# Kernel optimization log

Measured on AMD Instinct MI355X. Metric: run time of the kernel, lower is better.

Reference implementation:

```python
import jax, jax.numpy as jnp
import numpy as np

B, L, H, C = 1, 512, 1024, 2


def setup_inputs() -> dict:
    key = jax.random.key(0)
    k1, k2, k3 = jax.random.split(key, 3)
    lm_output = jax.random.normal(k1, (B, L, H), dtype=jnp.float32)
    # torch Linear weight layout: [out_features, in_features]
    W1 = jax.random.normal(k2, (H, 2 * H), dtype=jnp.float32) * 0.02
    b1 = jnp.zeros((H,), dtype=jnp.float32)
    W2 = jax.random.normal(k3, (C, H), dtype=jnp.float32) * 0.02
    b2 = jnp.zeros((C,), dtype=jnp.float32)
    return {"lm_output": lm_output, "W1": W1, "b1": b1, "W2": W2, "b2": b2}


def reference(lm_output, W1, b1, W2, b2):
    # pair_emb[b,i,j] = concat(lm_output[b,j], lm_output[b,i])
    # Linear(concat(a,b)) decomposes: split W1 into the halves acting on each part.
    Wa = W1[:, :H]  # acts on lm_output_a (the j / column token)
    Wb = W1[:, H:]  # acts on lm_output_b (the i / row token)
    a_proj = jnp.einsum('blh,oh->blo', lm_output, Wa)  # [B,L,H]
    b_proj = jnp.einsum('blh,oh->blo', lm_output, Wb)  # [B,L,H]
    # hidden[b,i,j] = tanh(a_proj[b,j] + b_proj[b,i] + b1)   -> [B,L,L,H]
    hidden = jnp.tanh(a_proj[:, None, :, :] + b_proj[:, :, None, :] + b1)
    # Dropout is identity at inference time.
    logits = jnp.einsum('bijh,ch->bijc', hidden, W2) + b2  # [B,L,L,C]
    logits = (logits + jnp.swapaxes(logits, 1, 2)) / 2.0
    return logits
```

## Files before the change

kernel.cpp:

```cpp
#include <hip/hip_runtime.h>
#include <hip/hip_bf16.h>

#define HH 1024
#define LL 512
#define NT 16
#define NTRI 136

typedef __attribute__((ext_vector_type(8))) short bf16x8;
typedef __attribute__((ext_vector_type(4))) float f32x4;

static constexpr float C_EXP = 2.8853900817779268f;

static __device__ __forceinline__ uint4 pack8(float4 a, float4 b) {
    union { uint4 u; __hip_bfloat162 h[4]; } r;
    r.h[0] = __float22bfloat162_rn(make_float2(a.x, a.y));
    r.h[1] = __float22bfloat162_rn(make_float2(a.z, a.w));
    r.h[2] = __float22bfloat162_rn(make_float2(b.x, b.y));
    r.h[3] = __float22bfloat162_rn(make_float2(b.z, b.w));
    return r.u;
}

__global__ __launch_bounds__(256) void convert_kernel(
    const float* __restrict__ lm, const float* __restrict__ W1,
    const float* __restrict__ W2,
    ushort* __restrict__ lm16, ushort* __restrict__ B16, float* __restrict__ wsum)
{
    const int b = blockIdx.x;
    if (b == 1280) {
        const int tid = threadIdx.x;
        if (tid < 128) {
            const int c = tid >> 6, l = tid & 63;
            float s = 0.f;
            for (int q = l; q < 256; q += 64) {
                const float4 v = *(const float4*)&W2[c * HH + q * 4];
                s += v.x + v.y + v.z + v.w;
            }
#pragma unroll
            for (int off = 32; off; off >>= 1) s += __shfl_down(s, off, 64);
            if (l == 0) wsum[c] = s;
        }
        return;
    }
    const int q = b * 256 + threadIdx.x;
    if (q < 65536) {
        const float4 a = *(const float4*)&lm[q * 8];
        const float4 c = *(const float4*)&lm[q * 8 + 4];
        ((uint4*)lm16)[q] = pack8(a, c);
    } else {
        const int p = q - 65536;
        const int n = p >> 7, k8 = (p & 127) * 8;
        const float* src = &W1[(n & 1023) * 2048 + (n >> 10) * 1024 + k8];
        ((uint4*)B16)[p] = pack8(*(const float4*)src, *(const float4*)(src + 4));
    }
}

__global__ __launch_bounds__(256, 4) void proj_mfma_kernel(
    const ushort* __restrict__ lm16, const ushort* __restrict__ B16,
    const float* __restrict__ b1, float* __restrict__ Ea, float* __restrict__ Eb)
{
    __shared__ ushort As[16][136];
    __shared__ ushort Bs[64][136];

    const int tid  = threadIdx.x;
    const int lane = tid & 63;
    const int w    = tid >> 6;
    const int linear = blockIdx.x;
    const int xcd  = linear & 7;
    const int idx  = linear >> 3;
    const int nbase = (xcd * 4 + (idx & 3)) * 64;
    const int mbase = (idx >> 2) * 16;
    const int wn   = w * 16;

    const int mrow = lane & 15;
    const int q8   = (lane >> 4) * 8;

    f32x4 acc = {0.f, 0.f, 0.f, 0.f};

    for (int kb = 0; kb < HH; kb += 128) {
        __syncthreads();
        {
            const int row = tid >> 4, c8 = (tid & 15) * 8;
            *(uint4*)&As[row][c8] = *(const uint4*)&lm16[(mbase + row) * HH + kb + c8];
            int p = tid;
#pragma unroll
            for (int it = 0; it < 4; ++it, p += 256) {
                const int br = p >> 4, bc8 = (p & 15) * 8;
                *(uint4*)&Bs[br][bc8] = *(const uint4*)&B16[(nbase + br) * HH + kb + bc8];
            }
        }
        __syncthreads();

#pragma unroll
        for (int s = 0; s < 4; ++s) {
            const bf16x8 a = *(const bf16x8*)&As[mrow][s * 32 + q8];
            const bf16x8 b = *(const bf16x8*)&Bs[wn + mrow][s * 32 + q8];
            acc = __builtin_amdgcn_mfma_f32_16x16x32_bf16(a, b, acc, 0, 0, 0);
        }
    }

    const int col = lane & 15;
    const int rq  = (lane >> 4) * 4;
    const int n_g = nbase + wn + col;
    const int m0  = mbase + rq;
    if (n_g < HH) {
        const float bb = b1[n_g];
#pragma unroll
        for (int r = 0; r < 4; ++r)
            Ea[(m0 + r) * HH + n_g] = __builtin_amdgcn_exp2f(C_EXP * (acc[r] + bb));
    } else {
#pragma unroll
        for (int r = 0; r < 4; ++r)
            Eb[(m0 + r) * HH + (n_g - HH)] = __builtin_amdgcn_exp2f(C_EXP * acc[r]);
    }
}

__global__ __launch_bounds__(256, 4) void pair_kernel(
    const float* __restrict__ Ea, const float* __restrict__ Eb,
    const float* __restrict__ W2, float* __restrict__ pbuf, int nz)
{
    __shared__ float eaj[32][68];
    __shared__ float eai[32][68];
    __shared__ float ebi[32][68];
    __shared__ float ebj[32][68];
    __shared__ float w0_s[256], w1_s[256];

    const int tid = threadIdx.x;
    const int tx  = tid & 15;
    const int ty  = tid >> 4;

    int tt = blockIdx.x, bi = 0, rem = NT;
    while (tt >= rem) { tt -= rem; --rem; ++bi; }
    const int bj    = bi + tt;
    const int ibase = bi * 32;
    const int jbase = bj * 32;
    const int slice = HH / nz;
    const int k0    = blockIdx.y * slice;

    if (tid < 128) {
        const int c = tid >> 6, l = tid & 63;
        float* ws = c ? w1_s : w0_s;
        for (int q = l; q < slice / 4; q += 64)
            ((float4*)ws)[q] = *(const float4*)&W2[c * HH + k0 + q * 4];
    }

    float acc[2][2][2] = {};

    for (int kb = 0; kb < slice; kb += 64) {
        __syncthreads();
        {
            int p = tid;
#pragma unroll
            for (int it = 0; it < 8; ++it, p += 256) {
                const int tile = p >> 9;
                const int row  = (p >> 4) & 31;
                const int c4   = p & 15;
                float4 v;
                if      (tile == 0) v = *(const float4*)&Ea[(jbase + row) * HH + k0 + kb + c4 * 4];
                else if (tile == 1) v = *(const float4*)&Ea[(ibase + row) * HH + k0 + kb + c4 * 4];
                else if (tile == 2) v = *(const float4*)&Eb[(ibase + row) * HH + k0 + kb + c4 * 4];
                else                v = *(const float4*)&Eb[(jbase + row) * HH + k0 + kb + c4 * 4];
                if      (tile == 0) *(float4*)&eaj[row][c4 * 4] = v;
                else if (tile == 1) *(float4*)&eai[row][c4 * 4] = v;
                else if (tile == 2) *(float4*)&ebi[row][c4 * 4] = v;
                else                *(float4*)&ebj[row][c4 * 4] = v;
            }
        }
        __syncthreads();

#pragma unroll 4
        for (int h4 = 0; h4 < 16; ++h4) {
            const float4 Aj0 = *(const float4*)&eaj[tx][h4 * 4];
            const float4 Aj1 = *(const float4*)&eaj[tx + 16][h4 * 4];
            const float4 Bi0 = *(const float4*)&ebi[ty][h4 * 4];
            const float4 Bi1 = *(const float4*)&ebi[ty + 16][h4 * 4];
            const float4 Ai0 = *(const float4*)&eai[ty][h4 * 4];
            const float4 Ai1 = *(const float4*)&eai[ty + 16][h4 * 4];
            const float4 Bj0 = *(const float4*)&ebj[tx][h4 * 4];
            const float4 Bj1 = *(const float4*)&ebj[tx + 16][h4 * 4];
            const float4 w0  = *(const float4*)&w0_s[kb + h4 * 4];
            const float4 w1  = *(const float4*)&w1_s[kb + h4 * 4];

#define DO_H(AJ0, AJ1, BI0, BI1, AI0, AI1, BJ0, BJ1, W0V, W1V)        \
            {                                                          \
                const float d00 = __builtin_fmaf((BI0), (AJ0), 1.f);   \
                const float d01 = __builtin_fmaf((BI0), (AJ1), 1.f);   \
                const float d10 = __builtin_fmaf((BI1), (AJ0), 1.f);   \
                const float d11 = __builtin_fmaf((BI1), (AJ1), 1.f);   \
                const float e00 = __builtin_fmaf((AI0), (BJ0), 1.f);   \
                const float e01 = __builtin_fmaf((AI0), (BJ1), 1.f);   \
                const float e10 = __builtin_fmaf((AI1), (BJ0), 1.f);   \
                const float e11 = __builtin_fmaf((AI1), (BJ1), 1.f);   \
                const float dp0 = d00 * d01, dp1 = d10 * d11;          \
                const float DR  = __builtin_amdgcn_rcpf(dp0 * dp1);    \
                const float dq0 = DR * dp1, dq1 = DR * dp0;            \
                const float rd00 = dq0 * d01, rd01 = dq0 * d00;        \
                const float rd10 = dq1 * d11, rd11 = dq1 * d10;        \
                const float ep0 = e00 * e01, ep1 = e10 * e11;          \
                const float ER  = __builtin_amdgcn_rcpf(ep0 * ep1);    \
                const float eq0 = ER * ep1, eq1 = ER * ep0;            \
                const float re00 = eq0 * e01, re01 = eq0 * e00;        \
                const float re10 = eq1 * e11, re11 = eq1 * e10;        \
                const float u00 = rd00 + re00, u01 = rd01 + re01;      \
                const float u10 = rd10 + re10, u11 = rd11 + re11;      \
                acc[0][0][0] = __builtin_fmaf(u00, (W0V), acc[0][0][0]); \
                acc[0][0][1] = __builtin_fmaf(u00, (W1V), acc[0][0][1]); \
                acc[0][1][0] = __builtin_fmaf(u01, (W0V), acc[0][1][0]); \
                acc[0][1][1] = __builtin_fmaf(u01, (W1V), acc[0][1][1]); \
                acc[1][0][0] = __builtin_fmaf(u10, (W0V), acc[1][0][0]); \
                acc[1][0][1] = __builtin_fmaf(u10, (W1V), acc[1][0][1]); \
                acc[1][1][0] = __builtin_fmaf(u11, (W0V), acc[1][1][0]); \
                acc[1][1][1] = __builtin_fmaf(u11, (W1V), acc[1][1][1]); \
            }
            DO_H(Aj0.x, Aj1.x, Bi0.x, Bi1.x, Ai0.x, Ai1.x, Bj0.x, Bj1.x, w0.x, w1.x)
            DO_H(Aj0.y, Aj1.y, Bi0.y, Bi1.y, Ai0.y, Ai1.y, Bj0.y, Bj1.y, w0.y, w1.y)
            DO_H(Aj0.z, Aj1.z, Bi0.z, Bi1.z, Ai0.z, Ai1.z, Bj0.z, Bj1.z, w0.z, w1.z)
            DO_H(Aj0.w, Aj1.w, Bi0.w, Bi1.w, Ai0.w, Ai1.w, Bj0.w, Bj1.w, w0.w, w1.w)
#undef DO_H
        }
    }

    float* pb = pbuf + ((size_t)blockIdx.y * NTRI + blockIdx.x) * 2048;
#pragma unroll
    for (int ii = 0; ii < 2; ++ii)
#pragma unroll
        for (int jj = 0; jj < 2; ++jj) {
            const int li = ty + ii * 16, lj = tx + jj * 16;
            *(float2*)&pb[(li * 32 + lj) * 2] =
                make_float2(acc[ii][jj][0], acc[ii][jj][1]);
        }
}

__global__ __launch_bounds__(256) void combine_kernel(
    const float* __restrict__ pbuf, const float* __restrict__ b2,
    const float* __restrict__ wsum, float* __restrict__ out, int nz)
{
    const int idx   = blockIdx.x * 256 + threadIdx.x;
    const int t     = idx >> 11;
    const int local = idx & 2047;
    int tt = t, bi = 0, rem = NT;
    while (tt >= rem) { tt -= rem; --rem; ++bi; }
    const int bj = bi + tt;

    float s = 0.f;
    for (int z = 0; z < nz; ++z)
        s += pbuf[((size_t)z * NTRI + t) * 2048 + local];

    const int li = local >> 6;
    const int lj = (local >> 1) & 31;
    const int c  = local & 1;
    const float v = wsum[c] + b2[c] - s;

    const int i = bi * 32 + li;
    const int j = bj * 32 + lj;
    out[(i * LL + j) * 2 + c] = v;
    out[(j * LL + i) * 2 + c] = v;
}

extern "C" void kernel_launch(void* const* d_in, const int* in_sizes, int n_in,
                              void* d_out, int out_size, void* d_ws, size_t ws_size,
                              hipStream_t stream)
{
    const float* lm = (const float*)d_in[0];
    const float* W1 = (const float*)d_in[1];
    const float* b1 = (const float*)d_in[2];
    const float* W2 = (const float*)d_in[3];
    const float* b2 = (const float*)d_in[4];
    float* out = (float*)d_out;

    char* ws = (char*)d_ws;
    float*  Ea   = (float*)ws;
    float*  Eb   = (float*)(ws + (2u << 20));
    ushort* lm16 = (ushort*)(ws + (4u << 20));
    ushort* B16  = (ushort*)(ws + (5u << 20));
    float*  wsum = (float*)(ws + (9u << 20));
    float*  pbuf = (float*)(ws + (9u << 20) + 256);

    const size_t base = (9u << 20) + 256;
    int nz = 16;
    while (nz > 4 && base + (size_t)nz * NTRI * 2048 * 4 > ws_size) nz >>= 1;

    convert_kernel<<<1281, 256, 0, stream>>>(lm, W1, W2, lm16, B16, wsum);
    proj_mfma_kernel<<<1024, 256, 0, stream>>>(lm16, B16, b1, Ea, Eb);
    pair_kernel<<<dim3(NTRI, nz), 256, 0, stream>>>(Ea, Eb, W2, pbuf, nz);
    combine_kernel<<<(NTRI * 2048) / 256, 256, 0, stream>>>(pbuf, b2, wsum, out, nz);
}
```

Measured before the change: 130.8 us.

## Store interleaved bf16 exp projections and drop LDS from projection GEMM

The projection kernel now loads MFMA fragments straight from global memory with no LDS staging or barriers, and each wave computes its own 16x16 tile. The exp(2x) outputs for the a and b halves are packed as bf16 pairs into one interleaved 32-bit array. The pair kernel therefore loads two tiles instead of four and unpacks them with shifts and masks, which halves its global and LDS traffic and lets occupancy rise to 6 blocks. The split-K factor drops from 16 to 8, giving fewer partial buffers but less parallelism, and the bf16 exponentials lose some accuracy.

```diff
diff --git a/kernel.cpp b/kernel.cpp
--- a/kernel.cpp
+++ b/kernel.cpp
@@ -10,6 +10,12 @@
 typedef __attribute__((ext_vector_type(4))) float f32x4;
 
 static constexpr float C_EXP = 2.8853900817779268f;
+
+static __device__ __forceinline__ ushort f2bf(float f) {
+    unsigned u = __builtin_bit_cast(unsigned, f);
+    u += 0x7fffu + ((u >> 16) & 1u);
+    return (ushort)(u >> 16);
+}
 
 static __device__ __forceinline__ uint4 pack8(float4 a, float4 b) {
     union { uint4 u; __hip_bfloat162 h[4]; } r;
@@ -56,72 +62,53 @@
 
 __global__ __launch_bounds__(256, 4) void proj_mfma_kernel(
     const ushort* __restrict__ lm16, const ushort* __restrict__ B16,
-    const float* __restrict__ b1, float* __restrict__ Ea, float* __restrict__ Eb)
-{
-    __shared__ ushort As[16][136];
-    __shared__ ushort Bs[64][136];
-
+    const float* __restrict__ b1, uint* __restrict__ Eab)
+{
     const int tid  = threadIdx.x;
     const int lane = tid & 63;
     const int w    = tid >> 6;
-    const int linear = blockIdx.x;
-    const int xcd  = linear & 7;
-    const int idx  = linear >> 3;
-    const int nbase = (xcd * 4 + (idx & 3)) * 64;
-    const int mbase = (idx >> 2) * 16;
-    const int wn   = w * 16;
-
-    const int mrow = lane & 15;
+    const int b    = blockIdx.x;
+    const int xcd  = b & 7, s = b >> 3;
+    const int m_tile = s >> 2;
+    const int n_tile = xcd * 16 + (s & 3) * 4 + w;
+    const int mbase = m_tile * 16;
+    const int nbase = n_tile * 16;
+
+    const int frow = lane & 15;
     const int q8   = (lane >> 4) * 8;
 
+    const ushort* ap = &lm16[(mbase + frow) * HH + q8];
+    const ushort* bp = &B16[(nbase + frow) * HH + q8];
+
     f32x4 acc = {0.f, 0.f, 0.f, 0.f};
-
-    for (int kb = 0; kb < HH; kb += 128) {
-        __syncthreads();
-        {
-            const int row = tid >> 4, c8 = (tid & 15) * 8;
-            *(uint4*)&As[row][c8] = *(const uint4*)&lm16[(mbase + row) * HH + kb + c8];
-            int p = tid;
-#pragma unroll
-            for (int it = 0; it < 4; ++it, p += 256) {
-                const int br = p >> 4, bc8 = (p & 15) * 8;
-                *(uint4*)&Bs[br][bc8] = *(const uint4*)&B16[(nbase + br) * HH + kb + bc8];
-            }
-        }
-        __syncthreads();
-
-#pragma unroll
-        for (int s = 0; s < 4; ++s) {
-            const bf16x8 a = *(const bf16x8*)&As[mrow][s * 32 + q8];
-            const bf16x8 b = *(const bf16x8*)&Bs[wn + mrow][s * 32 + q8];
-            acc = __builtin_amdgcn_mfma_f32_16x16x32_bf16(a, b, acc, 0, 0, 0);
-        }
-    }
-
-    const int col = lane & 15;
-    const int rq  = (lane >> 4) * 4;
-    const int n_g = nbase + wn + col;
-    const int m0  = mbase + rq;
-    if (n_g < HH) {
-        const float bb = b1[n_g];
-#pragma unroll
-        for (int r = 0; r < 4; ++r)
-            Ea[(m0 + r) * HH + n_g] = __builtin_amdgcn_exp2f(C_EXP * (acc[r] + bb));
-    } else {
-#pragma unroll
-        for (int r = 0; r < 4; ++r)
-            Eb[(m0 + r) * HH + (n_g - HH)] = __builtin_amdgcn_exp2f(C_EXP * acc[r]);
-    }
-}
-
-__global__ __launch_bounds__(256, 4) void pair_kernel(
-    const float* __restrict__ Ea, const float* __restrict__ Eb,
-    const float* __restrict__ W2, float* __restrict__ pbuf, int nz)
-{
-    __shared__ float eaj[32][68];
-    __shared__ float eai[32][68];
-    __shared__ float ebi[32][68];
-    __shared__ float ebj[32][68];
+#pragma unroll 8
+    for (int kb = 0; kb < HH; kb += 32) {
+        const bf16x8 a  = *(const bf16x8*)(ap + kb);
+        const bf16x8 bb = *(const bf16x8*)(bp + kb);
+        acc = __builtin_amdgcn_mfma_f32_16x16x32_bf16(a, bb, acc, 0, 0, 0);
+    }
+
+    const int col  = lane & 15;
+    const int rq   = (lane >> 4) * 4;
+    const int n_g  = nbase + col;
+    const int m0   = mbase + rq;
+    const int half = n_g >> 10;
+    const int nn   = n_g & 1023;
+    const float bb1 = half ? 0.f : b1[n_g & 1023];
+    ushort* eo = (ushort*)Eab;
+#pragma unroll
+    for (int r = 0; r < 4; ++r) {
+        const float e = __builtin_amdgcn_exp2f(C_EXP * (acc[r] + bb1));
+        eo[((m0 + r) * HH + nn) * 2 + half] = f2bf(e);
+    }
+}
+
+__global__ __launch_bounds__(256, 6) void pair_kernel(
+    const uint* __restrict__ Eab, const float* __restrict__ W2,
+    float* __restrict__ pbuf, int nz)
+{
+    __shared__ uint jt[32][68];
+    __shared__ uint it_[32][68];
     __shared__ float w0_s[256], w1_s[256];
 
     const int tid = threadIdx.x;
@@ -136,11 +123,12 @@
     const int slice = HH / nz;
     const int k0    = blockIdx.y * slice;
 
-    if (tid < 128) {
-        const int c = tid >> 6, l = tid & 63;
-        float* ws = c ? w1_s : w0_s;
-        for (int q = l; q < slice / 4; q += 64)
-            ((float4*)ws)[q] = *(const float4*)&W2[c * HH + k0 + q * 4];
+    {
+        const int nf4 = slice >> 2;
+        if (tid < 2 * nf4) {
+            const int c = tid >= nf4, q = tid - c * nf4;
+            ((float4*)(c ? w1_s : w0_s))[q] = *(const float4*)&W2[c * HH + k0 + q * 4];
+        }
     }
 
     float acc[2][2][2] = {};
@@ -150,46 +138,43 @@
         {
             int p = tid;
 #pragma unroll
-            for (int it = 0; it < 8; ++it, p += 256) {
-                const int tile = p >> 9;
-                const int row  = (p >> 4) & 31;
-                const int c4   = p & 15;
-                float4 v;
-                if      (tile == 0) v = *(const float4*)&Ea[(jbase + row) * HH + k0 + kb + c4 * 4];
-                else if (tile == 1) v = *(const float4*)&Ea[(ibase + row) * HH + k0 + kb + c4 * 4];
-                else if (tile == 2) v = *(const float4*)&Eb[(ibase + row) * HH + k0 + kb + c4 * 4];
-                else                v = *(const float4*)&Eb[(jbase + row) * HH + k0 + kb + c4 * 4];
-                if      (tile == 0) *(float4*)&eaj[row][c4 * 4] = v;
-                else if (tile == 1) *(float4*)&eai[row][c4 * 4] = v;
-                else if (tile == 2) *(float4*)&ebi[row][c4 * 4] = v;
-                else                *(float4*)&ebj[row][c4 * 4] = v;
+            for (int it2 = 0; it2 < 4; ++it2, p += 256) {
+                const int tile = p >> 9, row = (p >> 4) & 31, c4 = p & 15;
+                const int rb = tile ? ibase : jbase;
+                const uint4 v = *(const uint4*)&Eab[(rb + row) * HH + k0 + kb + c4 * 4];
+                if (tile) *(uint4*)&it_[row][c4 * 4] = v;
+                else      *(uint4*)&jt[row][c4 * 4] = v;
             }
         }
         __syncthreads();
 
 #pragma unroll 4
         for (int h4 = 0; h4 < 16; ++h4) {
-            const float4 Aj0 = *(const float4*)&eaj[tx][h4 * 4];
-            const float4 Aj1 = *(const float4*)&eaj[tx + 16][h4 * 4];
-            const float4 Bi0 = *(const float4*)&ebi[ty][h4 * 4];
-            const float4 Bi1 = *(const float4*)&ebi[ty + 16][h4 * 4];
-            const float4 Ai0 = *(const float4*)&eai[ty][h4 * 4];
-            const float4 Ai1 = *(const float4*)&eai[ty + 16][h4 * 4];
-            const float4 Bj0 = *(const float4*)&ebj[tx][h4 * 4];
-            const float4 Bj1 = *(const float4*)&ebj[tx + 16][h4 * 4];
-            const float4 w0  = *(const float4*)&w0_s[kb + h4 * 4];
-            const float4 w1  = *(const float4*)&w1_s[kb + h4 * 4];
-
-#define DO_H(AJ0, AJ1, BI0, BI1, AI0, AI1, BJ0, BJ1, W0V, W1V)        \
+            const uint4 J0 = *(const uint4*)&jt[tx][h4 * 4];
+            const uint4 J1 = *(const uint4*)&jt[tx + 16][h4 * 4];
+            const uint4 I0 = *(const uint4*)&it_[ty][h4 * 4];
+            const uint4 I1 = *(const uint4*)&it_[ty + 16][h4 * 4];
+            const float4 w0 = *(const float4*)&w0_s[kb + h4 * 4];
+            const float4 w1 = *(const float4*)&w1_s[kb + h4 * 4];
+
+#define DO_H(UJ0, UJ1, UI0, UI1, W0V, W1V)                             \
             {                                                          \
-                const float d00 = __builtin_fmaf((BI0), (AJ0), 1.f);   \
-                const float d01 = __builtin_fmaf((BI0), (AJ1), 1.f);   \
-                const float d10 = __builtin_fmaf((BI1), (AJ0), 1.f);   \
-                const float d11 = __builtin_fmaf((BI1), (AJ1), 1.f);   \
-                const float e00 = __builtin_fmaf((AI0), (BJ0), 1.f);   \
-                const float e01 = __builtin_fmaf((AI0), (BJ1), 1.f);   \
-                const float e10 = __builtin_fmaf((AI1), (BJ0), 1.f);   \
-                const float e11 = __builtin_fmaf((AI1), (BJ1), 1.f);   \
+                const float Aj0 = __builtin_bit_cast(float, (UJ0) << 16);          \
+                const float Bj0 = __builtin_bit_cast(float, (UJ0) & 0xffff0000u);  \
+                const float Aj1 = __builtin_bit_cast(float, (UJ1) << 16);          \
+                const float Bj1 = __builtin_bit_cast(float, (UJ1) & 0xffff0000u);  \
+                const float Ai0 = __builtin_bit_cast(float, (UI0) << 16);          \
+                const float Bi0 = __builtin_bit_cast(float, (UI0) & 0xffff0000u);  \
+                const float Ai1 = __builtin_bit_cast(float, (UI1) << 16);          \
+                const float Bi1 = __builtin_bit_cast(float, (UI1) & 0xffff0000u);  \
+                const float d00 = __builtin_fmaf(Bi0, Aj0, 1.f);       \
+                const float d01 = __builtin_fmaf(Bi0, Aj1, 1.f);       \
+                const float d10 = __builtin_fmaf(Bi1, Aj0, 1.f);       \
+                const float d11 = __builtin_fmaf(Bi1, Aj1, 1.f);       \
+                const float e00 = __builtin_fmaf(Ai0, Bj0, 1.f);       \
+                const float e01 = __builtin_fmaf(Ai0, Bj1, 1.f);       \
+                const float e10 = __builtin_fmaf(Ai1, Bj0, 1.f);       \
+                const float e11 = __builtin_fmaf(Ai1, Bj1, 1.f);       \
                 const float dp0 = d00 * d01, dp1 = d10 * d11;          \
                 const float DR  = __builtin_amdgcn_rcpf(dp0 * dp1);    \
                 const float dq0 = DR * dp1, dq1 = DR * dp0;            \
@@ -211,10 +196,10 @@
                 acc[1][1][0] = __builtin_fmaf(u11, (W0V), acc[1][1][0]); \
                 acc[1][1][1] = __builtin_fmaf(u11, (W1V), acc[1][1][1]); \
             }
-            DO_H(Aj0.x, Aj1.x, Bi0.x, Bi1.x, Ai0.x, Ai1.x, Bj0.x, Bj1.x, w0.x, w1.x)
-            DO_H(Aj0.y, Aj1.y, Bi0.y, Bi1.y, Ai0.y, Ai1.y, Bj0.y, Bj1.y, w0.y, w1.y)
-            DO_H(Aj0.z, Aj1.z, Bi0.z, Bi1.z, Ai0.z, Ai1.z, Bj0.z, Bj1.z, w0.z, w1.z)
-            DO_H(Aj0.w, Aj1.w, Bi0.w, Bi1.w, Ai0.w, Ai1.w, Bj0.w, Bj1.w, w0.w, w1.w)
+            DO_H(J0.x, J1.x, I0.x, I1.x, w0.x, w1.x)
+            DO_H(J0.y, J1.y, I0.y, I1.y, w0.y, w1.y)
+            DO_H(J0.z, J1.z, I0.z, I1.z, w0.z, w1.z)
+            DO_H(J0.w, J1.w, I0.w, I1.w, w0.w, w1.w)
 #undef DO_H
         }
     }
@@ -268,19 +253,18 @@
     float* out = (float*)d_out;
 
     char* ws = (char*)d_ws;
-    float*  Ea   = (float*)ws;
-    float*  Eb   = (float*)(ws + (2u << 20));
-    ushort* lm16 = (ushort*)(ws + (4u << 20));
-    ushort* B16  = (ushort*)(ws + (5u << 20));
-    float*  wsum = (float*)(ws + (9u << 20));
-    float*  pbuf = (float*)(ws + (9u << 20) + 256);
-
-    const size_t base = (9u << 20) + 256;
-    int nz = 16;
-    while (nz > 4 && base + (size_t)nz * NTRI * 2048 * 4 > ws_size) nz >>= 1;
+    uint*   Eab  = (uint*)ws;
+    ushort* lm16 = (ushort*)(ws + (2u << 20));
+    ushort* B16  = (ushort*)(ws + (3u << 20));
+    float*  wsum = (float*)(ws + (7u << 20));
+    float*  pbuf = (float*)(ws + (7u << 20) + 256);
+
+    const size_t base = (7u << 20) + 256;
+    int nz = 8;
+    while (nz > 2 && base + (size_t)nz * NTRI * 2048 * 4 > ws_size) nz >>= 1;
 
     convert_kernel<<<1281, 256, 0, stream>>>(lm, W1, W2, lm16, B16, wsum);
-    proj_mfma_kernel<<<1024, 256, 0, stream>>>(lm16, B16, b1, Ea, Eb);
-    pair_kernel<<<dim3(NTRI, nz), 256, 0, stream>>>(Ea, Eb, W2, pbuf, nz);
+    proj_mfma_kernel<<<1024, 256, 0, stream>>>(lm16, B16, b1, Eab);
+    pair_kernel<<<dim3(NTRI, nz), 256, 0, stream>>>(Eab, W2, pbuf, nz);
     combine_kernel<<<(NTRI * 2048) / 256, 256, 0, stream>>>(pbuf, b2, wsum, out, nz);
 }
```

Result: slower. 164.6 us (+25.8%).

## Retile projection GEMM to 64x128 blocks and transpose-combine via shared memory

Applied to the files above, without the earlier changes.

The projection GEMM moves from 16x64 tiles over 1024 blocks to 64x128 tiles over a 16x8 grid. Each wave now holds eight accumulators so every A fragment is reused across eight MFMAs, cutting global and LDS traffic per flop. The combine kernel assigns one block per triangle tile and stages values in shared memory so the mirrored (transposed) output writes are coalesced instead of strided. The W2 slice load in the pair kernel is also spread across more threads. The trade-off is far fewer proj blocks (128), which may leave many CUs idle on a large GPU.

```diff
diff --git a/kernel.cpp b/kernel.cpp
--- a/kernel.cpp
+++ b/kernel.cpp
@@ -54,63 +54,71 @@
     }
 }
 
-__global__ __launch_bounds__(256, 4) void proj_mfma_kernel(
+__global__ __launch_bounds__(256) void proj_mfma_kernel(
     const ushort* __restrict__ lm16, const ushort* __restrict__ B16,
     const float* __restrict__ b1, float* __restrict__ Ea, float* __restrict__ Eb)
 {
-    __shared__ ushort As[16][136];
-    __shared__ ushort Bs[64][136];
+    __shared__ ushort As[64][72];
+    __shared__ ushort Bs[128][72];
 
     const int tid  = threadIdx.x;
     const int lane = tid & 63;
     const int w    = tid >> 6;
-    const int linear = blockIdx.x;
-    const int xcd  = linear & 7;
-    const int idx  = linear >> 3;
-    const int nbase = (xcd * 4 + (idx & 3)) * 64;
-    const int mbase = (idx >> 2) * 16;
-    const int wn   = w * 16;
-
-    const int mrow = lane & 15;
+    const int nbase = blockIdx.x * 128;
+    const int mbase = blockIdx.y * 64;
+    const int wm   = w * 16;
+
+    const int frow = lane & 15;
     const int q8   = (lane >> 4) * 8;
 
-    f32x4 acc = {0.f, 0.f, 0.f, 0.f};
-
-    for (int kb = 0; kb < HH; kb += 128) {
+    f32x4 acc[8] = {};
+
+    for (int kb = 0; kb < HH; kb += 64) {
         __syncthreads();
         {
-            const int row = tid >> 4, c8 = (tid & 15) * 8;
-            *(uint4*)&As[row][c8] = *(const uint4*)&lm16[(mbase + row) * HH + kb + c8];
             int p = tid;
 #pragma unroll
+            for (int it = 0; it < 2; ++it, p += 256) {
+                const int row = p >> 3, c8 = (p & 7) * 8;
+                *(uint4*)&As[row][c8] = *(const uint4*)&lm16[(mbase + row) * HH + kb + c8];
+            }
+            p = tid;
+#pragma unroll
             for (int it = 0; it < 4; ++it, p += 256) {
-                const int br = p >> 4, bc8 = (p & 15) * 8;
-                *(uint4*)&Bs[br][bc8] = *(const uint4*)&B16[(nbase + br) * HH + kb + bc8];
+                const int row = p >> 3, c8 = (p & 7) * 8;
+                *(uint4*)&Bs[row][c8] = *(const uint4*)&B16[(nbase + row) * HH + kb + c8];
             }
         }
         __syncthreads();
 
 #pragma unroll
-        for (int s = 0; s < 4; ++s) {
-            const bf16x8 a = *(const bf16x8*)&As[mrow][s * 32 + q8];
-            const bf16x8 b = *(const bf16x8*)&Bs[wn + mrow][s * 32 + q8];
-            acc = __builtin_amdgcn_mfma_f32_16x16x32_bf16(a, b, acc, 0, 0, 0);
+        for (int s = 0; s < 2; ++s) {
+            const bf16x8 a = *(const bf16x8*)&As[wm + frow][s * 32 + q8];
+#pragma unroll
+            for (int nf = 0; nf < 8; ++nf) {
+                const bf16x8 bb = *(const bf16x8*)&Bs[nf * 16 + frow][s * 32 + q8];
+                acc[nf] = __builtin_amdgcn_mfma_f32_16x16x32_bf16(a, bb, acc[nf], 0, 0, 0);
+            }
         }
     }
 
     const int col = lane & 15;
     const int rq  = (lane >> 4) * 4;
-    const int n_g = nbase + wn + col;
-    const int m0  = mbase + rq;
-    if (n_g < HH) {
-        const float bb = b1[n_g];
-#pragma unroll
-        for (int r = 0; r < 4; ++r)
-            Ea[(m0 + r) * HH + n_g] = __builtin_amdgcn_exp2f(C_EXP * (acc[r] + bb));
-    } else {
-#pragma unroll
-        for (int r = 0; r < 4; ++r)
-            Eb[(m0 + r) * HH + (n_g - HH)] = __builtin_amdgcn_exp2f(C_EXP * acc[r]);
+    const int m0  = mbase + wm + rq;
+    const bool isA = nbase < HH;
+#pragma unroll
+    for (int nf = 0; nf < 8; ++nf) {
+        const int nn = (nbase + nf * 16 + col) & 1023;
+        if (isA) {
+            const float bb = b1[nn];
+#pragma unroll
+            for (int r = 0; r < 4; ++r)
+                Ea[(m0 + r) * HH + nn] = __builtin_amdgcn_exp2f(C_EXP * (acc[nf][r] + bb));
+        } else {
+#pragma unroll
+            for (int r = 0; r < 4; ++r)
+                Eb[(m0 + r) * HH + nn] = __builtin_amdgcn_exp2f(C_EXP * acc[nf][r]);
+        }
     }
 }
 
@@ -136,11 +144,12 @@
     const int slice = HH / nz;
     const int k0    = blockIdx.y * slice;
 
-    if (tid < 128) {
-        const int c = tid >> 6, l = tid & 63;
-        float* ws = c ? w1_s : w0_s;
-        for (int q = l; q < slice / 4; q += 64)
-            ((float4*)ws)[q] = *(const float4*)&W2[c * HH + k0 + q * 4];
+    {
+        const int nf4 = slice >> 2;
+        if (tid < 2 * nf4) {
+            const int c = tid >= nf4, q = tid - c * nf4;
+            ((float4*)(c ? w1_s : w0_s))[q] = *(const float4*)&W2[c * HH + k0 + q * 4];
+        }
     }
 
     float acc[2][2][2] = {};
@@ -234,26 +243,39 @@
     const float* __restrict__ pbuf, const float* __restrict__ b2,
     const float* __restrict__ wsum, float* __restrict__ out, int nz)
 {
-    const int idx   = blockIdx.x * 256 + threadIdx.x;
-    const int t     = idx >> 11;
-    const int local = idx & 2047;
+    __shared__ float ts[2][32][33];
+
+    const int tid = threadIdx.x;
+    const int t   = blockIdx.x;
     int tt = t, bi = 0, rem = NT;
     while (tt >= rem) { tt -= rem; --rem; ++bi; }
     const int bj = bi + tt;
 
-    float s = 0.f;
-    for (int z = 0; z < nz; ++z)
-        s += pbuf[((size_t)z * NTRI + t) * 2048 + local];
-
-    const int li = local >> 6;
-    const int lj = (local >> 1) & 31;
-    const int c  = local & 1;
-    const float v = wsum[c] + b2[c] - s;
-
-    const int i = bi * 32 + li;
-    const int j = bj * 32 + lj;
-    out[(i * LL + j) * 2 + c] = v;
-    out[(j * LL + i) * 2 + c] = v;
+    const float base0 = wsum[0] + b2[0];
+    const float base1 = wsum[1] + b2[1];
+
+#pragma unroll
+    for (int k = 0; k < 8; ++k) {
+        const int local = k * 256 + tid;
+        float s = 0.f;
+        for (int z = 0; z < nz; ++z)
+            s += pbuf[((size_t)z * NTRI + t) * 2048 + local];
+        const int li = local >> 6;
+        const int lj = (local >> 1) & 31;
+        const int c  = local & 1;
+        const float v = (c ? base1 : base0) - s;
+        ts[c][li][lj] = v;
+        out[((bi * 32 + li) * LL + bj * 32 + lj) * 2 + c] = v;
+    }
+    __syncthreads();
+#pragma unroll
+    for (int k = 0; k < 8; ++k) {
+        const int local = k * 256 + tid;
+        const int lj = local >> 6;
+        const int li = (local >> 1) & 31;
+        const int c  = local & 1;
+        out[((bj * 32 + lj) * LL + bi * 32 + li) * 2 + c] = ts[c][li][lj];
+    }
 }
 
 extern "C" void kernel_launch(void* const* d_in, const int* in_sizes, int n_in,
@@ -280,7 +302,7 @@
     while (nz > 4 && base + (size_t)nz * NTRI * 2048 * 4 > ws_size) nz >>= 1;
 
     convert_kernel<<<1281, 256, 0, stream>>>(lm, W1, W2, lm16, B16, wsum);
-    proj_mfma_kernel<<<1024, 256, 0, stream>>>(lm16, B16, b1, Ea, Eb);
+    proj_mfma_kernel<<<dim3(16, 8), 256, 0, stream>>>(lm16, B16, b1, Ea, Eb);
     pair_kernel<<<dim3(NTRI, nz), 256, 0, stream>>>(Ea, Eb, W2, pbuf, nz);
-    combine_kernel<<<(NTRI * 2048) / 256, 256, 0, stream>>>(pbuf, b2, wsum, out, nz);
-}
+    combine_kernel<<<NTRI, 256, 0, stream>>>(pbuf, b2, wsum, out, nz);
+}
```

Measured after the change: 185.2 us. 41.6% more time.
